# Performance work log

Hardware: AMD Instinct MI355X
Metric: run time of the kernel (lower is better)

## Reference

```python
import jax, jax.numpy as jnp
import numpy as np

B, C, H, W = 16, 512, 32, 32
GROUPS = 8
EPS = 1e-5


def setup_inputs() -> dict:
    key = jax.random.key(0)
    ks = jax.random.split(key, 7)
    s = 1.0 / np.sqrt(C)
    return {
        "x": jax.random.normal(ks[0], (B, C, H, W), dtype=jnp.float32),
        "gamma": jnp.ones((C,), dtype=jnp.float32),
        "beta": jnp.zeros((C,), dtype=jnp.float32),
        "w_qkv": jax.random.normal(ks[1], (3 * C, C), dtype=jnp.float32) * s,
        "b_qkv": jnp.zeros((3 * C,), dtype=jnp.float32),
        "w_proj": jax.random.normal(ks[2], (C, C), dtype=jnp.float32) * s,
        "b_proj": jnp.zeros((C,), dtype=jnp.float32),
    }


def group_norm(x, gamma, beta):
    b, c, h, w = x.shape
    xg = x.reshape(b, GROUPS, c // GROUPS, h, w)
    mean = xg.mean(axis=(2, 3, 4), keepdims=True)
    var = xg.var(axis=(2, 3, 4), keepdims=True)
    xn = ((xg - mean) * jax.lax.rsqrt(var + EPS)).reshape(b, c, h, w)
    return xn * gamma[None, :, None, None] + beta[None, :, None, None]


def reference(x, gamma, beta, w_qkv, b_qkv, w_proj, b_proj):
    b, c, h, w = x.shape
    n = h * w
    hn = group_norm(x, gamma, beta)
    # 1x1 conv == channel matmul: [3C, C] x [B, C, N] -> [B, 3C, N]
    qkv = jnp.einsum('oc,bcn->bon', w_qkv, hn.reshape(b, c, n)) + b_qkv[None, :, None]
    q, k, v = jnp.split(qkv, 3, axis=1)  # each [B, C, N]
    scale = c ** (-0.5)
    # scores [B, N, N]: q^T k
    attn = jax.nn.softmax(jnp.einsum('bcn,bcm->bnm', q, k) * scale, axis=-1)
    out = jnp.einsum('bnm,bcm->bcn', attn, v)  # [B, C, N]
    proj = jnp.einsum('oc,bcn->bon', w_proj, out) + b_proj[None, :, None]
    return x + proj.reshape(b, c, h, w)
```

## Files before the change

kernel.cpp:

```cpp
#include <hip/hip_runtime.h>


#define BATCH 16
#define CCH 512
#define NSP 1024
#define EPSV 1e-5f
#define BK 32
#define HT 4096

typedef short bf16x8 __attribute__((ext_vector_type(8)));
typedef float f32x4 __attribute__((ext_vector_type(4)));

__device__ __forceinline__ unsigned short f2bf(float f) {
    unsigned int u = __float_as_uint(f);
    u += 0x7FFF + ((u >> 16) & 1);
    return (unsigned short)(u >> 16);
}

__device__ __forceinline__ void glds16(const void* g, void* l) {
    __builtin_amdgcn_global_load_lds(
        (const __attribute__((address_space(1))) unsigned int*)g,
        (__attribute__((address_space(3))) unsigned int*)l, 16, 0, 0);
}

#define XCD_MAP(GX_LOG2, PER, xv, yv, bv)                 \
    const int lin_ = blockIdx.x;                          \
    const int xcd_ = lin_ & 7;                            \
    int slot_ = lin_ >> 3;                                \
    const int hi_ = (slot_ >= (PER)) ? 1 : 0;             \
    const int bv = xcd_ + 8 * hi_;                        \
    slot_ -= hi_ * (PER);                                 \
    const int xv = slot_ & ((1 << (GX_LOG2)) - 1);        \
    const int yv = slot_ >> (GX_LOG2);

__device__ __forceinline__ void gemm128_loop(
    const unsigned short* __restrict__ Ag, const unsigned short* __restrict__ Bg,
    int astr, int bstr, int ktot, short* Al, short* Bl, f32x4* acc) {
    const int t = threadIdx.x;
    const int w = t >> 6, lane = t & 63;
    const int wr = (w >> 1) * 64, wc = (w & 1) * 64;
    const int fr = lane & 15;
    const int fsw = (((lane >> 4) ^ (fr & 3)) * 8);
    const int r0 = t >> 2;
    const int kc = (((t & 3) ^ (r0 & 3)) * 8);
    const unsigned short* Ap0 = Ag + (size_t)r0 * astr + kc;
    const unsigned short* Ap1 = Ag + (size_t)(r0 + 64) * astr + kc;
    const unsigned short* Bp0 = Bg + (size_t)r0 * bstr + kc;
    const unsigned short* Bp1 = Bg + (size_t)(r0 + 64) * bstr + kc;
    short* Alw = Al + w * 512;
    short* Blw = Bl + w * 512;
    for (int k0 = 0; k0 < ktot; k0 += 64) {
        glds16(Ap0 + k0, Alw);
        glds16(Ap1 + k0, Alw + 2048);
        glds16(Ap0 + k0 + 32, Alw + HT);
        glds16(Ap1 + k0 + 32, Alw + HT + 2048);
        glds16(Bp0 + k0, Blw);
        glds16(Bp1 + k0, Blw + 2048);
        glds16(Bp0 + k0 + 32, Blw + HT);
        glds16(Bp1 + k0 + 32, Blw + HT + 2048);
        __syncthreads();
#pragma unroll
        for (int h = 0; h < 2; h++) {
            const short* Ab = Al + h * HT;
            const short* Bb = Bl + h * HT;
            bf16x8 af[4], bfr[4];
#pragma unroll
            for (int mi = 0; mi < 4; mi++)
                af[mi] = *(const bf16x8*)(Ab + (wr + mi * 16 + fr) * BK + fsw);
#pragma unroll
            for (int ni = 0; ni < 4; ni++)
                bfr[ni] = *(const bf16x8*)(Bb + (wc + ni * 16 + fr) * BK + fsw);
#pragma unroll
            for (int mi = 0; mi < 4; mi++)
#pragma unroll
                for (int ni = 0; ni < 4; ni++)
                    acc[mi * 4 + ni] = __builtin_amdgcn_mfma_f32_16x16x32_bf16(
                        af[mi], bfr[ni], acc[mi * 4 + ni], 0, 0, 0);
        }
        __syncthreads();
    }
}

#define EPI_SETUP()                                          \
    const int t = threadIdx.x, lane = t & 63, w = t >> 6;    \
    const int wr = (w >> 1) * 64, wc = (w & 1) * 64;         \
    const int fr = lane & 15, rr0 = (lane >> 4) * 4;

#define ACC_INIT(acc)                                        \
    f32x4 acc[16];                                           \
    _Pragma("unroll") for (int i = 0; i < 16; i++)           \
        acc[i] = (f32x4){0.f, 0.f, 0.f, 0.f};

__global__ __launch_bounds__(256) void setup_k(
    const float* __restrict__ x, float* __restrict__ stats,
    const float* __restrict__ wa, unsigned short* __restrict__ oa, int na4,
    const float* __restrict__ wb, unsigned short* __restrict__ ob, int nb4,
    float* __restrict__ Lsum) {
    const int t = threadIdx.x;
    if (blockIdx.x < 128) {
        const int bg = blockIdx.x;
        const float4* xp = (const float4*)(x + (size_t)bg * 65536);
        float s = 0.f, q = 0.f;
#pragma unroll
        for (int i = 0; i < 64; i++) {
            float4 v = xp[t + i * 256];
            s += v.x + v.y + v.z + v.w;
            q += v.x * v.x + v.y * v.y + v.z * v.z + v.w * v.w;
        }
#pragma unroll
        for (int off = 32; off; off >>= 1) {
            s += __shfl_down(s, off);
            q += __shfl_down(q, off);
        }
        __shared__ float rs[4], rq[4];
        const int wave = t >> 6, lane = t & 63;
        if (lane == 0) { rs[wave] = s; rq[wave] = q; }
        __syncthreads();
        if (t == 0) {
            float S = rs[0] + rs[1] + rs[2] + rs[3];
            float Q = rq[0] + rq[1] + rq[2] + rq[3];
            const float inv = 1.f / 65536.f;
            float mean = S * inv;
            float var = Q * inv - mean * mean;
            stats[bg * 2] = mean;
            stats[bg * 2 + 1] = rsqrtf(var + EPSV);
        }
    } else if (blockIdx.x < 1152) {
        int i = (blockIdx.x - 128) * 256 + t;
        const float* src;
        unsigned short* dst;
        int j;
        if (i < na4) { src = wa; dst = oa; j = i; }
        else { j = i - na4; if (j >= nb4) return; src = wb; dst = ob; }
        float4 v = ((const float4*)src)[j];
        ushort4 o;
        o.x = f2bf(v.x); o.y = f2bf(v.y); o.z = f2bf(v.z); o.w = f2bf(v.w);
        ((ushort4*)dst)[j] = o;
    } else {
        int i = (blockIdx.x - 1152) * 256 + t;
        ((float4*)Lsum)[i] = (float4){0.f, 0.f, 0.f, 0.f};
    }
}

__global__ __launch_bounds__(256) void gn_tr_k(
    const float* __restrict__ x, const float* __restrict__ gamma,
    const float* __restrict__ beta, const float* __restrict__ stats,
    unsigned short* __restrict__ hn_t) {
    const int nt = blockIdx.x, ct = blockIdx.y, b = blockIdx.z;
    __shared__ __align__(16) unsigned short T[64 * 72];
    const int t = threadIdx.x;
    const float mean = stats[(b * 8 + ct) * 2];
    const float rstd = stats[(b * 8 + ct) * 2 + 1];
    const int cl = t >> 2, nc = t & 3;
    const int c = ct * 64 + cl;
    const float ga = gamma[c] * rstd;
    const float be = beta[c] - mean * ga;
    const float4* xp = (const float4*)(x + ((size_t)b * CCH + c) * NSP + nt * 64);
#pragma unroll
    for (int j = 0; j < 4; j++) {
        float4 v = xp[nc * 4 + j];
        int n = nc * 16 + j * 4;
        T[(n + 0) * 72 + cl] = f2bf(v.x * ga + be);
        T[(n + 1) * 72 + cl] = f2bf(v.y * ga + be);
        T[(n + 2) * 72 + cl] = f2bf(v.z * ga + be);
        T[(n + 3) * 72 + cl] = f2bf(v.w * ga + be);
    }
    __syncthreads();
    const int nl = t >> 2, cc = t & 3;
    unsigned short* dst = hn_t + ((size_t)b * NSP + nt * 64 + nl) * CCH + ct * 64 + cc * 16;
    const unsigned short* src = T + nl * 72 + cc * 16;
    *(uint4*)dst = *(const uint4*)src;
    *(uint4*)(dst + 8) = *(const uint4*)(src + 8);
}

__global__ __launch_bounds__(256) void gemm_qkv_k(
    const unsigned short* __restrict__ hn_t, const unsigned short* __restrict__ wq,
    const float* __restrict__ bq, unsigned short* __restrict__ QKt,
    unsigned short* __restrict__ Vb) {
    __shared__ __align__(16) short Al[2 * HT], Bl[2 * HT];
    XCD_MAP(3, 96, xb, y, b);
    const int ntc = xb * 128;
    ACC_INIT(acc);
    if (y < 8) {
        const int mt = y * 128;
        gemm128_loop(hn_t + ((size_t)b * NSP + mt) * CCH,
                     wq + (size_t)ntc * CCH, CCH, CCH, CCH, Al, Bl, acc);
        unsigned short* Ob = QKt + (size_t)b * NSP * 1024;
        EPI_SETUP();
#pragma unroll
        for (int ni = 0; ni < 4; ni++) {
            int col = ntc + wc + ni * 16 + fr;
            float bias = bq[col];
#pragma unroll
            for (int mi = 0; mi < 4; mi++) {
                int row = mt + wr + mi * 16 + rr0;
#pragma unroll
                for (int r = 0; r < 4; r++)
                    Ob[(size_t)(row + r) * 1024 + col] = f2bf(acc[mi * 4 + ni][r] + bias);
            }
        }
    } else {
        const int mt = (y - 8) * 128;
        gemm128_loop(wq + (size_t)(1024 + mt) * CCH,
                     hn_t + ((size_t)b * NSP + ntc) * CCH, CCH, CCH, CCH, Al, Bl, acc);
        unsigned short* Ob = Vb + (size_t)b * CCH * NSP;
        EPI_SETUP();
#pragma unroll
        for (int mi = 0; mi < 4; mi++) {
            int row = mt + wr + mi * 16 + rr0;
#pragma unroll
            for (int r = 0; r < 4; r++) {
                float bias = bq[1024 + row + r];
#pragma unroll
                for (int ni = 0; ni < 4; ni++) {
                    int col = ntc + wc + ni * 16 + fr;
                    Ob[(size_t)(row + r) * NSP + col] = f2bf(acc[mi * 4 + ni][r] + bias);
                }
            }
        }
    }
}

__global__ __launch_bounds__(256) void gemm_scores_k(
    const unsigned short* __restrict__ QKt, unsigned short* __restrict__ expS,
    float* __restrict__ Lsum) {
    __shared__ __align__(16) short Al[2 * HT], Bl[2 * HT];
    XCD_MAP(3, 64, xb, yb, b);
    const int nt = xb * 128, mt = yb * 128;
    const unsigned short* base = QKt + (size_t)b * NSP * 1024;
    ACC_INIT(acc);
    gemm128_loop(base + (size_t)mt * 1024, base + (size_t)nt * 1024 + 512,
                 1024, 1024, 512, Al, Bl, acc);
    unsigned short* Ob = expS + (size_t)b * NSP * NSP;
    float* Ls = Lsum + (size_t)b * NSP;
    const float scale = 0.044194173824159216f;
    EPI_SETUP();
#pragma unroll
    for (int mi = 0; mi < 4; mi++) {
#pragma unroll
        for (int r = 0; r < 4; r++) {
            const int row = mt + wr + mi * 16 + rr0 + r;
            float rs = 0.f;
#pragma unroll
            for (int ni = 0; ni < 4; ni++) {
                int col = nt + wc + ni * 16 + fr;
                float e = __expf(acc[mi * 4 + ni][r] * scale);
                Ob[(size_t)row * NSP + col] = f2bf(e);
                rs += e;
            }
            rs += __shfl_xor(rs, 1);
            rs += __shfl_xor(rs, 2);
            rs += __shfl_xor(rs, 4);
            rs += __shfl_xor(rs, 8);
            if (fr == 0) atomicAdd(&Ls[row], rs);
        }
    }
}

__global__ __launch_bounds__(256) void gemm_pv_k(
    const unsigned short* __restrict__ expS, const unsigned short* __restrict__ Vb,
    const float* __restrict__ Lsum, unsigned short* __restrict__ At) {
    __shared__ __align__(16) short Al[2 * HT], Bl[2 * HT];
    XCD_MAP(2, 32, xb, yb, b);
    const int ntc = xb * 128, mt = yb * 128;
    ACC_INIT(acc);
    gemm128_loop(expS + ((size_t)b * NSP + mt) * NSP,
                 Vb + ((size_t)b * CCH + ntc) * NSP, NSP, NSP, NSP, Al, Bl, acc);
    unsigned short* Ob = At + (size_t)b * NSP * CCH;
    const float* Ls = Lsum + (size_t)b * NSP;
    EPI_SETUP();
#pragma unroll
    for (int mi = 0; mi < 4; mi++) {
        int row = mt + wr + mi * 16 + rr0;
#pragma unroll
        for (int r = 0; r < 4; r++) {
            float inv = __builtin_amdgcn_rcpf(Ls[row + r]);
#pragma unroll
            for (int ni = 0; ni < 4; ni++) {
                int col = ntc + wc + ni * 16 + fr;
                Ob[(size_t)(row + r) * CCH + col] = f2bf(acc[mi * 4 + ni][r] * inv);
            }
        }
    }
}

__global__ __launch_bounds__(256) void gemm_proj_k(
    const unsigned short* __restrict__ At, const unsigned short* __restrict__ wp,
    const float* __restrict__ bp, const float* __restrict__ x,
    float* __restrict__ out) {
    __shared__ __align__(16) short Al[2 * HT], Bl[2 * HT];
    XCD_MAP(3, 32, xb, yb, b);
    const int nt = xb * 128, mt = yb * 128;
    ACC_INIT(acc);
    gemm128_loop(wp + (size_t)mt * CCH, At + ((size_t)b * NSP + nt) * CCH,
                 CCH, CCH, CCH, Al, Bl, acc);
    const size_t bbase = (size_t)b * CCH * NSP;
    EPI_SETUP();
#pragma unroll
    for (int mi = 0; mi < 4; mi++) {
        int row = mt + wr + mi * 16 + rr0;
#pragma unroll
        for (int r = 0; r < 4; r++) {
            float bias = bp[row + r];
#pragma unroll
            for (int ni = 0; ni < 4; ni++) {
                int col = nt + wc + ni * 16 + fr;
                size_t idx = bbase + (size_t)(row + r) * NSP + col;
                out[idx] = x[idx] + bias + acc[mi * 4 + ni][r];
            }
        }
    }
}

extern "C" void kernel_launch(void* const* d_in, const int* in_sizes, int n_in,
                              void* d_out, int out_size, void* d_ws, size_t ws_size,
                              hipStream_t stream) {
    const float* x = (const float*)d_in[0];
    const float* gamma = (const float*)d_in[1];
    const float* beta = (const float*)d_in[2];
    const float* w_qkv = (const float*)d_in[3];
    const float* b_qkv = (const float*)d_in[4];
    const float* w_proj = (const float*)d_in[5];
    const float* b_proj = (const float*)d_in[6];
    float* out = (float*)d_out;

    char* ws = (char*)d_ws;
    const size_t MB = 1048576;
    unsigned short* wqkv_bf = (unsigned short*)ws;
    unsigned short* wproj_bf = (unsigned short*)(ws + 1572864);
    float* stats = (float*)(ws + 2 * MB);
    float* Lsum = (float*)(ws + 2 * MB + 65536);
    unsigned short* hn_t = (unsigned short*)(ws + 4 * MB);
    unsigned short* At = hn_t;
    unsigned short* QKt = (unsigned short*)(ws + 24 * MB);
    unsigned short* Vb = (unsigned short*)(ws + 60 * MB);
    unsigned short* expS = (unsigned short*)(ws + 80 * MB);

    setup_k<<<1168, 256, 0, stream>>>(x, stats, w_qkv, wqkv_bf, 196608,
                                      w_proj, wproj_bf, 65536, Lsum);
    gn_tr_k<<<dim3(16, 8, BATCH), 256, 0, stream>>>(x, gamma, beta, stats, hn_t);
    gemm_qkv_k<<<1536, 256, 0, stream>>>(hn_t, wqkv_bf, b_qkv, QKt, Vb);
    gemm_scores_k<<<1024, 256, 0, stream>>>(QKt, expS, Lsum);
    gemm_pv_k<<<512, 256, 0, stream>>>(expS, Vb, Lsum, At);
    gemm_proj_k<<<512, 256, 0, stream>>>(At, wproj_bf, b_proj, x, out);
}
```

Before: 211.2 us.

## Fold Q and K projections into one combined weight for the score GEMM

```diff
diff --git a/kernel.cpp b/kernel.cpp
--- a/kernel.cpp
+++ b/kernel.cpp
@@ -15,6 +15,10 @@
     unsigned int u = __float_as_uint(f);
     u += 0x7FFF + ((u >> 16) & 1);
     return (unsigned short)(u >> 16);
+}
+
+__device__ __forceinline__ float bf2f(unsigned short h) {
+    return __uint_as_float(((unsigned int)h) << 16);
 }
 
 __device__ __forceinline__ void glds16(const void* g, void* l) {
@@ -95,10 +99,15 @@
     const float* __restrict__ x, float* __restrict__ stats,
     const float* __restrict__ wa, unsigned short* __restrict__ oa, int na4,
     const float* __restrict__ wb, unsigned short* __restrict__ ob, int nb4,
-    float* __restrict__ Lsum) {
+    float* __restrict__ Lsum, const float* __restrict__ bqv,
+    unsigned short* __restrict__ wq_t, unsigned short* __restrict__ wk_t,
+    float* __restrict__ wu, float* __restrict__ wv, float* __restrict__ c0p) {
     const int t = threadIdx.x;
-    if (blockIdx.x < 128) {
-        const int bg = blockIdx.x;
+    __shared__ float rs[4], rq[4];
+    __shared__ __align__(16) unsigned short Tt[64 * 72];
+    const int bx = blockIdx.x;
+    if (bx < 128) {
+        const int bg = bx;
         const float4* xp = (const float4*)(x + (size_t)bg * 65536);
         float s = 0.f, q = 0.f;
 #pragma unroll
@@ -112,7 +121,6 @@
             s += __shfl_down(s, off);
             q += __shfl_down(q, off);
         }
-        __shared__ float rs[4], rq[4];
         const int wave = t >> 6, lane = t & 63;
         if (lane == 0) { rs[wave] = s; rq[wave] = q; }
         __syncthreads();
@@ -125,8 +133,8 @@
             stats[bg * 2] = mean;
             stats[bg * 2 + 1] = rsqrtf(var + EPSV);
         }
-    } else if (blockIdx.x < 1152) {
-        int i = (blockIdx.x - 128) * 256 + t;
+    } else if (bx < 1152) {
+        int i = (bx - 128) * 256 + t;
         const float* src;
         unsigned short* dst;
         int j;
@@ -136,19 +144,88 @@
         ushort4 o;
         o.x = f2bf(v.x); o.y = f2bf(v.y); o.z = f2bf(v.z); o.w = f2bf(v.w);
         ((ushort4*)dst)[j] = o;
+    } else if (bx < 1200) {
+        int i = (bx - 1152) * 256 + t;
+        ((float4*)Lsum)[i] = (float4){0.f, 0.f, 0.f, 0.f};
+    } else if (bx < 1328) {
+        const int r = bx - 1200;
+        const int sel = r >> 6;
+        const float* src = wa + (size_t)sel * 512 * 512;
+        unsigned short* dst = sel ? wk_t : wq_t;
+        const int to = ((r & 63) >> 3) * 64, tc = ((r & 63) & 7) * 64;
+        const int ol = t >> 2, cs = t & 3;
+#pragma unroll
+        for (int j = 0; j < 4; j++) {
+            float4 v = *(const float4*)(src + (size_t)(to + ol) * 512 + tc + cs * 16 + j * 4);
+            int c = cs * 16 + j * 4;
+            Tt[(c + 0) * 72 + ol] = f2bf(v.x);
+            Tt[(c + 1) * 72 + ol] = f2bf(v.y);
+            Tt[(c + 2) * 72 + ol] = f2bf(v.z);
+            Tt[(c + 3) * 72 + ol] = f2bf(v.w);
+        }
+        __syncthreads();
+        const int cl = t >> 2, os = t & 3;
+        unsigned short* d = dst + (size_t)(tc + cl) * 512 + to + os * 16;
+        const unsigned short* s2 = Tt + cl * 72 + os * 16;
+        *(uint4*)d = *(const uint4*)s2;
+        *(uint4*)(d + 8) = *(const uint4*)(s2 + 8);
+    } else if (bx < 1332) {
+        const int r = bx - 1328;
+        const int isv = r >> 1;
+        const int c = (r & 1) * 256 + t;
+        const float* src = wa + (size_t)isv * 512 * 512;
+        const float* bsr = bqv + (isv ? 0 : 512);
+        float s = 0.f;
+        for (int o = 0; o < 512; o += 4) {
+            s += src[(size_t)(o + 0) * 512 + c] * bsr[o + 0];
+            s += src[(size_t)(o + 1) * 512 + c] * bsr[o + 1];
+            s += src[(size_t)(o + 2) * 512 + c] * bsr[o + 2];
+            s += src[(size_t)(o + 3) * 512 + c] * bsr[o + 3];
+        }
+        (isv ? wv : wu)[c] = s;
     } else {
-        int i = (blockIdx.x - 1152) * 256 + t;
-        ((float4*)Lsum)[i] = (float4){0.f, 0.f, 0.f, 0.f};
+        float s = bqv[t] * bqv[512 + t] + bqv[256 + t] * bqv[768 + t];
+#pragma unroll
+        for (int off = 32; off; off >>= 1) s += __shfl_down(s, off);
+        if ((t & 63) == 0) rs[t >> 6] = s;
+        __syncthreads();
+        if (t == 0) c0p[0] = rs[0] + rs[1] + rs[2] + rs[3];
     }
 }
 
 __global__ __launch_bounds__(256) void gn_tr_k(
     const float* __restrict__ x, const float* __restrict__ gamma,
     const float* __restrict__ beta, const float* __restrict__ stats,
-    unsigned short* __restrict__ hn_t) {
-    const int nt = blockIdx.x, ct = blockIdx.y, b = blockIdx.z;
-    __shared__ __align__(16) unsigned short T[64 * 72];
+    unsigned short* __restrict__ hn_t,
+    const unsigned short* __restrict__ wk_t, const unsigned short* __restrict__ wq_t,
+    unsigned short* __restrict__ wqkb,
+    const float* __restrict__ wu, const float* __restrict__ wv,
+    float* __restrict__ u, float* __restrict__ v) {
+    __shared__ __align__(16) short SM[4 * HT];
+    const int lin = blockIdx.x;
     const int t = threadIdx.x;
+    if (lin < 16) {
+        const int jt = (lin >> 2) * 128, ct2 = (lin & 3) * 128;
+        ACC_INIT(acc);
+        gemm128_loop(wk_t + (size_t)jt * 512, wq_t + (size_t)ct2 * 512,
+                     512, 512, 512, SM, SM + 2 * HT, acc);
+        EPI_SETUP();
+#pragma unroll
+        for (int ni = 0; ni < 4; ni++) {
+            int col = ct2 + wc + ni * 16 + fr;
+#pragma unroll
+            for (int mi = 0; mi < 4; mi++) {
+                int row = jt + wr + mi * 16 + rr0;
+#pragma unroll
+                for (int r = 0; r < 4; r++)
+                    wqkb[(size_t)(row + r) * 512 + col] = f2bf(acc[mi * 4 + ni][r]);
+            }
+        }
+        return;
+    }
+    const int l2 = lin - 16;
+    const int nt = l2 & 15, ct = (l2 >> 4) & 7, b = l2 >> 7;
+    unsigned short* T = (unsigned short*)SM;
     const float mean = stats[(b * 8 + ct) * 2];
     const float rstd = stats[(b * 8 + ct) * 2 + 1];
     const int cl = t >> 2, nc = t & 3;
@@ -158,12 +235,12 @@
     const float4* xp = (const float4*)(x + ((size_t)b * CCH + c) * NSP + nt * 64);
 #pragma unroll
     for (int j = 0; j < 4; j++) {
-        float4 v = xp[nc * 4 + j];
+        float4 vx = xp[nc * 4 + j];
         int n = nc * 16 + j * 4;
-        T[(n + 0) * 72 + cl] = f2bf(v.x * ga + be);
-        T[(n + 1) * 72 + cl] = f2bf(v.y * ga + be);
-        T[(n + 2) * 72 + cl] = f2bf(v.z * ga + be);
-        T[(n + 3) * 72 + cl] = f2bf(v.w * ga + be);
+        T[(n + 0) * 72 + cl] = f2bf(vx.x * ga + be);
+        T[(n + 1) * 72 + cl] = f2bf(vx.y * ga + be);
+        T[(n + 2) * 72 + cl] = f2bf(vx.z * ga + be);
+        T[(n + 3) * 72 + cl] = f2bf(vx.w * ga + be);
     }
     __syncthreads();
     const int nl = t >> 2, cc = t & 3;
@@ -171,36 +248,53 @@
     const unsigned short* src = T + nl * 72 + cc * 16;
     *(uint4*)dst = *(const uint4*)src;
     *(uint4*)(dst + 8) = *(const uint4*)(src + 8);
-}
-
-__global__ __launch_bounds__(256) void gemm_qkv_k(
+    float pu = 0.f, pv = 0.f;
+    const int cbase = ct * 64 + cc * 16;
+#pragma unroll
+    for (int j = 0; j < 16; j++) {
+        float hv = bf2f(src[j]);
+        pu += hv * wu[cbase + j];
+        pv += hv * wv[cbase + j];
+    }
+    pu += __shfl_xor(pu, 1); pu += __shfl_xor(pu, 2);
+    pv += __shfl_xor(pv, 1); pv += __shfl_xor(pv, 2);
+    if (cc == 0) {
+        atomicAdd(&u[(size_t)b * NSP + nt * 64 + nl], pu);
+        atomicAdd(&v[(size_t)b * NSP + nt * 64 + nl], pv);
+    }
+}
+
+__global__ __launch_bounds__(256) void gemm_t1v_k(
     const unsigned short* __restrict__ hn_t, const unsigned short* __restrict__ wq,
-    const float* __restrict__ bq, unsigned short* __restrict__ QKt,
-    unsigned short* __restrict__ Vb) {
+    const unsigned short* __restrict__ wqkb, const float* __restrict__ bq,
+    unsigned short* __restrict__ T1, unsigned short* __restrict__ Vb) {
     __shared__ __align__(16) short Al[2 * HT], Bl[2 * HT];
-    XCD_MAP(3, 96, xb, y, b);
-    const int ntc = xb * 128;
+    const int lin = blockIdx.x, xcd = lin & 7;
+    int slot = lin >> 3;
+    const int hi = (slot >= 64) ? 1 : 0;
+    const int b = xcd + 8 * hi;
+    slot -= hi * 64;
     ACC_INIT(acc);
-    if (y < 8) {
-        const int mt = y * 128;
+    if (slot < 32) {
+        const int mt = (slot >> 2) * 128, jt = (slot & 3) * 128;
         gemm128_loop(hn_t + ((size_t)b * NSP + mt) * CCH,
-                     wq + (size_t)ntc * CCH, CCH, CCH, CCH, Al, Bl, acc);
-        unsigned short* Ob = QKt + (size_t)b * NSP * 1024;
+                     wqkb + (size_t)jt * 512, CCH, 512, CCH, Al, Bl, acc);
+        unsigned short* Ob = T1 + (size_t)b * NSP * 512;
         EPI_SETUP();
 #pragma unroll
         for (int ni = 0; ni < 4; ni++) {
-            int col = ntc + wc + ni * 16 + fr;
-            float bias = bq[col];
+            int col = jt + wc + ni * 16 + fr;
 #pragma unroll
             for (int mi = 0; mi < 4; mi++) {
                 int row = mt + wr + mi * 16 + rr0;
 #pragma unroll
                 for (int r = 0; r < 4; r++)
-                    Ob[(size_t)(row + r) * 1024 + col] = f2bf(acc[mi * 4 + ni][r] + bias);
+                    Ob[(size_t)(row + r) * 512 + col] = f2bf(acc[mi * 4 + ni][r]);
             }
         }
     } else {
-        const int mt = (y - 8) * 128;
+        const int s2 = slot - 32;
+        const int mt = (s2 >> 3) * 128, ntc = (s2 & 7) * 128;
         gemm128_loop(wq + (size_t)(1024 + mt) * CCH,
                      hn_t + ((size_t)b * NSP + ntc) * CCH, CCH, CCH, CCH, Al, Bl, acc);
         unsigned short* Ob = Vb + (size_t)b * CCH * NSP;
@@ -222,17 +316,21 @@
 }
 
 __global__ __launch_bounds__(256) void gemm_scores_k(
-    const unsigned short* __restrict__ QKt, unsigned short* __restrict__ expS,
-    float* __restrict__ Lsum) {
+    const unsigned short* __restrict__ T1, const unsigned short* __restrict__ hn_t,
+    unsigned short* __restrict__ expS, float* __restrict__ Lsum,
+    const float* __restrict__ u, const float* __restrict__ v,
+    const float* __restrict__ c0p) {
     __shared__ __align__(16) short Al[2 * HT], Bl[2 * HT];
     XCD_MAP(3, 64, xb, yb, b);
     const int nt = xb * 128, mt = yb * 128;
-    const unsigned short* base = QKt + (size_t)b * NSP * 1024;
     ACC_INIT(acc);
-    gemm128_loop(base + (size_t)mt * 1024, base + (size_t)nt * 1024 + 512,
-                 1024, 1024, 512, Al, Bl, acc);
+    gemm128_loop(T1 + ((size_t)b * NSP + mt) * 512,
+                 hn_t + ((size_t)b * NSP + nt) * CCH, 512, CCH, 512, Al, Bl, acc);
     unsigned short* Ob = expS + (size_t)b * NSP * NSP;
     float* Ls = Lsum + (size_t)b * NSP;
+    const float* ua = u + (size_t)b * NSP;
+    const float* va = v + (size_t)b * NSP;
+    const float c0v = c0p[0];
     const float scale = 0.044194173824159216f;
     EPI_SETUP();
 #pragma unroll
@@ -240,11 +338,12 @@
 #pragma unroll
         for (int r = 0; r < 4; r++) {
             const int row = mt + wr + mi * 16 + rr0 + r;
+            const float ur = ua[row] + c0v;
             float rs = 0.f;
 #pragma unroll
             for (int ni = 0; ni < 4; ni++) {
                 int col = nt + wc + ni * 16 + fr;
-                float e = __expf(acc[mi * 4 + ni][r] * scale);
+                float e = __expf((acc[mi * 4 + ni][r] + ur + va[col]) * scale);
                 Ob[(size_t)row * NSP + col] = f2bf(e);
                 rs += e;
             }
@@ -326,21 +425,32 @@
 
     char* ws = (char*)d_ws;
     const size_t MB = 1048576;
+    const size_t KB = 1024;
     unsigned short* wqkv_bf = (unsigned short*)ws;
     unsigned short* wproj_bf = (unsigned short*)(ws + 1572864);
     float* stats = (float*)(ws + 2 * MB);
-    float* Lsum = (float*)(ws + 2 * MB + 65536);
+    float* Lsum = (float*)(ws + 2 * MB + 64 * KB);
+    float* u = (float*)(ws + 2 * MB + 128 * KB);
+    float* v = (float*)(ws + 2 * MB + 192 * KB);
+    float* wu = (float*)(ws + 2 * MB + 256 * KB);
+    float* wv = (float*)(ws + 2 * MB + 260 * KB);
+    float* c0p = (float*)(ws + 2 * MB + 264 * KB);
+    unsigned short* wq_t = (unsigned short*)(ws + 2 * MB + 512 * KB);
+    unsigned short* wk_t = (unsigned short*)(ws + 3 * MB);
+    unsigned short* wqkb = (unsigned short*)(ws + 3 * MB + 512 * KB);
     unsigned short* hn_t = (unsigned short*)(ws + 4 * MB);
     unsigned short* At = hn_t;
-    unsigned short* QKt = (unsigned short*)(ws + 24 * MB);
+    unsigned short* T1 = (unsigned short*)(ws + 24 * MB);
     unsigned short* Vb = (unsigned short*)(ws + 60 * MB);
     unsigned short* expS = (unsigned short*)(ws + 80 * MB);
 
-    setup_k<<<1168, 256, 0, stream>>>(x, stats, w_qkv, wqkv_bf, 196608,
-                                      w_proj, wproj_bf, 65536, Lsum);
-    gn_tr_k<<<dim3(16, 8, BATCH), 256, 0, stream>>>(x, gamma, beta, stats, hn_t);
-    gemm_qkv_k<<<1536, 256, 0, stream>>>(hn_t, wqkv_bf, b_qkv, QKt, Vb);
-    gemm_scores_k<<<1024, 256, 0, stream>>>(QKt, expS, Lsum);
+    setup_k<<<1333, 256, 0, stream>>>(x, stats, w_qkv, wqkv_bf, 196608,
+                                      w_proj, wproj_bf, 65536, Lsum, b_qkv,
+                                      wq_t, wk_t, wu, wv, c0p);
+    gn_tr_k<<<2064, 256, 0, stream>>>(x, gamma, beta, stats, hn_t,
+                                      wk_t, wq_t, wqkb, wu, wv, u, v);
+    gemm_t1v_k<<<1024, 256, 0, stream>>>(hn_t, wqkv_bf, wqkb, b_qkv, T1, Vb);
+    gemm_scores_k<<<1024, 256, 0, stream>>>(T1, hn_t, expS, Lsum, u, v, c0p);
     gemm_pv_k<<<512, 256, 0, stream>>>(expS, Vb, Lsum, At);
     gemm_proj_k<<<512, 256, 0, stream>>>(At, wproj_bf, b_proj, x, out);
 }
```

New measurement: 225.5 us. 1.07x slower.

## Fold projection weight into V and fuse PV with output projection

Applied to the files above, without the earlier changes.

```diff
diff --git a/kernel.cpp b/kernel.cpp
--- a/kernel.cpp
+++ b/kernel.cpp
@@ -95,10 +95,14 @@
     const float* __restrict__ x, float* __restrict__ stats,
     const float* __restrict__ wa, unsigned short* __restrict__ oa, int na4,
     const float* __restrict__ wb, unsigned short* __restrict__ ob, int nb4,
-    float* __restrict__ Lsum) {
+    float* __restrict__ Lsum, const float* __restrict__ bqv,
+    unsigned short* __restrict__ wv_t, float* __restrict__ puv) {
     const int t = threadIdx.x;
-    if (blockIdx.x < 128) {
-        const int bg = blockIdx.x;
+    const int bx = blockIdx.x;
+    __shared__ float rs[4], rq[4];
+    __shared__ __align__(16) unsigned short Tt[64 * 72];
+    if (bx < 128) {
+        const int bg = bx;
         const float4* xp = (const float4*)(x + (size_t)bg * 65536);
         float s = 0.f, q = 0.f;
 #pragma unroll
@@ -112,7 +116,6 @@
             s += __shfl_down(s, off);
             q += __shfl_down(q, off);
         }
-        __shared__ float rs[4], rq[4];
         const int wave = t >> 6, lane = t & 63;
         if (lane == 0) { rs[wave] = s; rq[wave] = q; }
         __syncthreads();
@@ -125,8 +128,8 @@
             stats[bg * 2] = mean;
             stats[bg * 2 + 1] = rsqrtf(var + EPSV);
         }
-    } else if (blockIdx.x < 1152) {
-        int i = (blockIdx.x - 128) * 256 + t;
+    } else if (bx < 896) {
+        int i = (bx - 128) * 256 + t;
         const float* src;
         unsigned short* dst;
         int j;
@@ -136,19 +139,73 @@
         ushort4 o;
         o.x = f2bf(v.x); o.y = f2bf(v.y); o.z = f2bf(v.z); o.w = f2bf(v.w);
         ((ushort4*)dst)[j] = o;
+    } else if (bx < 912) {
+        int i = (bx - 896) * 256 + t;
+        ((float4*)Lsum)[i] = (float4){0.f, 0.f, 0.f, 0.f};
+    } else if (bx < 976) {
+        const int r = bx - 912;
+        const float* src = wa + (size_t)2 * 512 * 512;
+        const int to = (r >> 3) * 64, tc = (r & 7) * 64;
+        const int ol = t >> 2, cs = t & 3;
+#pragma unroll
+        for (int j = 0; j < 4; j++) {
+            float4 v = *(const float4*)(src + (size_t)(to + ol) * 512 + tc + cs * 16 + j * 4);
+            int c = cs * 16 + j * 4;
+            Tt[(c + 0) * 72 + ol] = f2bf(v.x);
+            Tt[(c + 1) * 72 + ol] = f2bf(v.y);
+            Tt[(c + 2) * 72 + ol] = f2bf(v.z);
+            Tt[(c + 3) * 72 + ol] = f2bf(v.w);
+        }
+        __syncthreads();
+        const int cl = t >> 2, os = t & 3;
+        unsigned short* d = wv_t + (size_t)(tc + cl) * 512 + to + os * 16;
+        const unsigned short* s2 = Tt + cl * 72 + os * 16;
+        *(uint4*)d = *(const uint4*)s2;
+        *(uint4*)(d + 8) = *(const uint4*)(s2 + 8);
     } else {
-        int i = (blockIdx.x - 1152) * 256 + t;
-        ((float4*)Lsum)[i] = (float4){0.f, 0.f, 0.f, 0.f};
+        const int o = (bx - 976) * 256 + t;
+        const float* wr_ = wb + (size_t)o * 512;
+        const float* bv = bqv + 1024;
+        float s = 0.f;
+        for (int vv = 0; vv < 512; vv += 4) {
+            s += wr_[vv] * bv[vv] + wr_[vv + 1] * bv[vv + 1]
+               + wr_[vv + 2] * bv[vv + 2] + wr_[vv + 3] * bv[vv + 3];
+        }
+        puv[o] = s;
     }
 }
 
 __global__ __launch_bounds__(256) void gn_tr_k(
     const float* __restrict__ x, const float* __restrict__ gamma,
     const float* __restrict__ beta, const float* __restrict__ stats,
-    unsigned short* __restrict__ hn_t) {
-    const int nt = blockIdx.x, ct = blockIdx.y, b = blockIdx.z;
-    __shared__ __align__(16) unsigned short T[64 * 72];
+    unsigned short* __restrict__ hn_t,
+    const unsigned short* __restrict__ wp_bf, const unsigned short* __restrict__ wv_t,
+    unsigned short* __restrict__ wpv_bf) {
+    __shared__ __align__(16) short SM[4 * HT];
+    const int lin = blockIdx.x;
     const int t = threadIdx.x;
+    if (lin < 16) {
+        const int ot = (lin >> 2) * 128, ct2 = (lin & 3) * 128;
+        ACC_INIT(acc);
+        gemm128_loop(wp_bf + (size_t)ot * 512, wv_t + (size_t)ct2 * 512,
+                     512, 512, 512, SM, SM + 2 * HT, acc);
+        EPI_SETUP();
+#pragma unroll
+        for (int ni = 0; ni < 4; ni++) {
+            int col = ct2 + wc + ni * 16 + fr;
+#pragma unroll
+            for (int mi = 0; mi < 4; mi++) {
+                int row = ot + wr + mi * 16 + rr0;
+#pragma unroll
+                for (int r = 0; r < 4; r++)
+                    wpv_bf[(size_t)(row + r) * 512 + col] = f2bf(acc[mi * 4 + ni][r]);
+            }
+        }
+        return;
+    }
+    const int l2 = lin - 16;
+    const int nt = l2 & 15, ct = (l2 >> 4) & 7, b = l2 >> 7;
+    unsigned short* T = (unsigned short*)SM;
     const float mean = stats[(b * 8 + ct) * 2];
     const float rstd = stats[(b * 8 + ct) * 2 + 1];
     const int cl = t >> 2, nc = t & 3;
@@ -173,10 +230,11 @@
     *(uint4*)(dst + 8) = *(const uint4*)(src + 8);
 }
 
-__global__ __launch_bounds__(256) void gemm_qkv_k(
+__global__ __launch_bounds__(256) void gemm_qku_k(
     const unsigned short* __restrict__ hn_t, const unsigned short* __restrict__ wq,
-    const float* __restrict__ bq, unsigned short* __restrict__ QKt,
-    unsigned short* __restrict__ Vb) {
+    const float* __restrict__ bq, const unsigned short* __restrict__ wpv_bf,
+    const float* __restrict__ puv, unsigned short* __restrict__ QKt,
+    unsigned short* __restrict__ Ub) {
     __shared__ __align__(16) short Al[2 * HT], Bl[2 * HT];
     XCD_MAP(3, 96, xb, y, b);
     const int ntc = xb * 128;
@@ -201,16 +259,16 @@
         }
     } else {
         const int mt = (y - 8) * 128;
-        gemm128_loop(wq + (size_t)(1024 + mt) * CCH,
-                     hn_t + ((size_t)b * NSP + ntc) * CCH, CCH, CCH, CCH, Al, Bl, acc);
-        unsigned short* Ob = Vb + (size_t)b * CCH * NSP;
+        gemm128_loop(wpv_bf + (size_t)mt * 512,
+                     hn_t + ((size_t)b * NSP + ntc) * CCH, 512, CCH, 512, Al, Bl, acc);
+        unsigned short* Ob = Ub + (size_t)b * CCH * NSP;
         EPI_SETUP();
 #pragma unroll
         for (int mi = 0; mi < 4; mi++) {
             int row = mt + wr + mi * 16 + rr0;
 #pragma unroll
             for (int r = 0; r < 4; r++) {
-                float bias = bq[1024 + row + r];
+                float bias = puv[row + r];
 #pragma unroll
                 for (int ni = 0; ni < 4; ni++) {
                     int col = ntc + wc + ni * 16 + fr;
@@ -257,56 +315,30 @@
     }
 }
 
-__global__ __launch_bounds__(256) void gemm_pv_k(
-    const unsigned short* __restrict__ expS, const unsigned short* __restrict__ Vb,
-    const float* __restrict__ Lsum, unsigned short* __restrict__ At) {
-    __shared__ __align__(16) short Al[2 * HT], Bl[2 * HT];
-    XCD_MAP(2, 32, xb, yb, b);
-    const int ntc = xb * 128, mt = yb * 128;
-    ACC_INIT(acc);
-    gemm128_loop(expS + ((size_t)b * NSP + mt) * NSP,
-                 Vb + ((size_t)b * CCH + ntc) * NSP, NSP, NSP, NSP, Al, Bl, acc);
-    unsigned short* Ob = At + (size_t)b * NSP * CCH;
-    const float* Ls = Lsum + (size_t)b * NSP;
-    EPI_SETUP();
-#pragma unroll
-    for (int mi = 0; mi < 4; mi++) {
-        int row = mt + wr + mi * 16 + rr0;
-#pragma unroll
-        for (int r = 0; r < 4; r++) {
-            float inv = __builtin_amdgcn_rcpf(Ls[row + r]);
-#pragma unroll
-            for (int ni = 0; ni < 4; ni++) {
-                int col = ntc + wc + ni * 16 + fr;
-                Ob[(size_t)(row + r) * CCH + col] = f2bf(acc[mi * 4 + ni][r] * inv);
-            }
-        }
-    }
-}
-
-__global__ __launch_bounds__(256) void gemm_proj_k(
-    const unsigned short* __restrict__ At, const unsigned short* __restrict__ wp,
-    const float* __restrict__ bp, const float* __restrict__ x,
-    float* __restrict__ out) {
+__global__ __launch_bounds__(256) void gemm_pu_k(
+    const unsigned short* __restrict__ Ub, const unsigned short* __restrict__ expS,
+    const float* __restrict__ Lsum, const float* __restrict__ x,
+    const float* __restrict__ bp, float* __restrict__ out) {
     __shared__ __align__(16) short Al[2 * HT], Bl[2 * HT];
     XCD_MAP(3, 32, xb, yb, b);
-    const int nt = xb * 128, mt = yb * 128;
+    const int nt = xb * 128, ot = yb * 128;
     ACC_INIT(acc);
-    gemm128_loop(wp + (size_t)mt * CCH, At + ((size_t)b * NSP + nt) * CCH,
-                 CCH, CCH, CCH, Al, Bl, acc);
+    gemm128_loop(Ub + ((size_t)b * CCH + ot) * NSP,
+                 expS + ((size_t)b * NSP + nt) * NSP, NSP, NSP, NSP, Al, Bl, acc);
+    const float* Ls = Lsum + (size_t)b * NSP;
     const size_t bbase = (size_t)b * CCH * NSP;
     EPI_SETUP();
 #pragma unroll
-    for (int mi = 0; mi < 4; mi++) {
-        int row = mt + wr + mi * 16 + rr0;
-#pragma unroll
-        for (int r = 0; r < 4; r++) {
-            float bias = bp[row + r];
-#pragma unroll
-            for (int ni = 0; ni < 4; ni++) {
-                int col = nt + wc + ni * 16 + fr;
+    for (int ni = 0; ni < 4; ni++) {
+        int col = nt + wc + ni * 16 + fr;
+        float invl = __builtin_amdgcn_rcpf(Ls[col]);
+#pragma unroll
+        for (int mi = 0; mi < 4; mi++) {
+            int row = ot + wr + mi * 16 + rr0;
+#pragma unroll
+            for (int r = 0; r < 4; r++) {
                 size_t idx = bbase + (size_t)(row + r) * NSP + col;
-                out[idx] = x[idx] + bias + acc[mi * 4 + ni][r];
+                out[idx] = x[idx] + bp[row + r] + acc[mi * 4 + ni][r] * invl;
             }
         }
     }
@@ -326,21 +358,26 @@
 
     char* ws = (char*)d_ws;
     const size_t MB = 1048576;
+    const size_t KB = 1024;
     unsigned short* wqkv_bf = (unsigned short*)ws;
     unsigned short* wproj_bf = (unsigned short*)(ws + 1572864);
     float* stats = (float*)(ws + 2 * MB);
-    float* Lsum = (float*)(ws + 2 * MB + 65536);
+    float* Lsum = (float*)(ws + 2 * MB + 64 * KB);
+    float* puv = (float*)(ws + 2 * MB + 128 * KB);
+    unsigned short* wv_t = (unsigned short*)(ws + 2 * MB + 256 * KB);
+    unsigned short* wpv_bf = (unsigned short*)(ws + 3 * MB);
     unsigned short* hn_t = (unsigned short*)(ws + 4 * MB);
-    unsigned short* At = hn_t;
     unsigned short* QKt = (unsigned short*)(ws + 24 * MB);
-    unsigned short* Vb = (unsigned short*)(ws + 60 * MB);
+    unsigned short* Ub = (unsigned short*)(ws + 60 * MB);
     unsigned short* expS = (unsigned short*)(ws + 80 * MB);
 
-    setup_k<<<1168, 256, 0, stream>>>(x, stats, w_qkv, wqkv_bf, 196608,
-                                      w_proj, wproj_bf, 65536, Lsum);
-    gn_tr_k<<<dim3(16, 8, BATCH), 256, 0, stream>>>(x, gamma, beta, stats, hn_t);
-    gemm_qkv_k<<<1536, 256, 0, stream>>>(hn_t, wqkv_bf, b_qkv, QKt, Vb);
+    setup_k<<<978, 256, 0, stream>>>(x, stats, w_qkv, wqkv_bf, 131072,
+                                     w_proj, wproj_bf, 65536, Lsum, b_qkv,
+                                     wv_t, puv);
+    gn_tr_k<<<2064, 256, 0, stream>>>(x, gamma, beta, stats, hn_t,
+                                      wproj_bf, wv_t, wpv_bf);
+    gemm_qku_k<<<1536, 256, 0, stream>>>(hn_t, wqkv_bf, b_qkv, wpv_bf, puv,
+                                         QKt, Ub);
     gemm_scores_k<<<1024, 256, 0, stream>>>(QKt, expS, Lsum);
-    gemm_pv_k<<<512, 256, 0, stream>>>(expS, Vb, Lsum, At);
-    gemm_proj_k<<<512, 256, 0, stream>>>(At, wproj_bf, b_proj, x, out);
-}
+    gemm_pu_k<<<512, 256, 0, stream>>>(Ub, expS, Lsum, x, b_proj, out);
+}
```

New measurement: 221.0 us. 1.05x slower.
